# Optimization experiments

Hardware: AMD Instinct MI355X
Metric: run time of the kernel (lower is better)

Reference implementation:

```python
import jax, jax.numpy as jnp
import numpy as np

FOUR_PI = 4.0 * np.pi
INF_CLAMP = 1e30


def setup_inputs() -> dict:
    key = jax.random.key(0)
    k1, k2, k3, k4 = jax.random.split(key, 4)
    B, N, M, S = 16, 2048, 16, 128
    pcl_transformed = jax.random.normal(k1, (B, N, M, 3), dtype=jnp.float32)
    primitive_points = jax.random.normal(k2, (B, M, S, 3), dtype=jnp.float32)
    size = jax.random.uniform(k3, (B, M, 3), dtype=jnp.float32, minval=0.05, maxval=1.0)
    probs = jax.random.uniform(k4, (B, M), dtype=jnp.float32)
    return {"pcl_transformed": pcl_transformed, "primitive_points": primitive_points,
            "size": size, "probs": probs}


def reference(pcl_transformed, primitive_points, size, probs):
    B, N, M, _ = pcl_transformed.shape
    S = primitive_points.shape[2]

    # diff: (B, M, S, N, 3); dist: (B, M, S, N)
    diff = primitive_points[:, :, :, None, :] - jnp.transpose(pcl_transformed, (0, 2, 1, 3))[:, :, None, :, :]
    dist = jnp.sum(diff * diff, axis=-1)

    # ---- pcl_to_prim loss (min over S, sort over M, stick-breaking cumprod) ----
    d1 = jnp.transpose(jnp.min(dist, axis=2), (0, 2, 1))  # (B, N, M)
    idx = jnp.argsort(d1, axis=-1)                         # (B, N, M)
    distance = jnp.take_along_axis(d1, idx, axis=-1)
    p = jnp.take_along_axis(jnp.broadcast_to(probs[:, None, :], (B, N, M)), idx, axis=-1)
    neg_cumprod = jnp.cumprod(1.0 - p, axis=-1)
    neg_cumprod = jnp.concatenate([jnp.ones_like(neg_cumprod[..., :1]), neg_cumprod[..., :-1]], axis=-1)
    minprob = p * neg_cumprod
    pcl_to_prim = jnp.einsum('bnm,bnm->', distance, minprob) / (B * N)

    # ---- prim_to_pcl loss (min over N, superquadric-area weighting) ----
    d2 = jnp.min(dist, axis=-1)                            # (B, M, S)
    d2 = jnp.where(d2 >= INF_CLAMP, 0.0, d2)
    s0, s1, s2 = size[..., 0], size[..., 1], size[..., 2]
    area = FOUR_PI * ((s0 * s1) ** 1.6 / 3 + (s0 * s2) ** 1.6 / 3 + (s1 * s2) ** 1.6 / 3) ** 0.625
    area = M * area / jnp.sum(area, axis=-1, keepdims=True)  # (B, M)
    prim_to_pcl = jnp.einsum('bm,bm,bm->', jnp.mean(d2, axis=-1), probs, area) / (B * M)

    # No regularizer types enabled -> regs == 0 (matches regularizer_type=[]).
    regs = jnp.zeros((), dtype=pcl_to_prim.dtype)
    total = 1.0 * pcl_to_prim + 1.0 * prim_to_pcl + regs
    return total, pcl_to_prim, prim_to_pcl, regs
```

## Files before the change

kernel.cpp:

```cpp
#include <hip/hip_runtime.h>
#include <math.h>

#define BB 16
#define NN 2048
#define MM 16
#define SS 128

__constant__ const float kFourPi = 12.566370614359172f;

__global__ __launch_bounds__(1024, 4) void fused_dist_kernel(
    const float* __restrict__ pcl,
    const float* __restrict__ prim,
    float* __restrict__ d1,
    float* __restrict__ d2sum,
    unsigned int* __restrict__ counter)
{
    const int bi  = blockIdx.x;
    const int b   = ((bi & 7) << 1) | (bi >> 7);
    const int m   = (bi >> 3) & 15;
    const int bm  = (b << 4) | m;
    const int tid = threadIdx.x;

    __shared__ float  Qx[NN], Qy[NN], Qz[NN], Qh[NN];
    __shared__ float4 Plds[SS];
    __shared__ float  d1s[4][NN];
    __shared__ float  wred[16][64];
    __shared__ float  rsum[4];

    if (bi == 0 && tid == 0)
        __hip_atomic_store(counter, 0u, __ATOMIC_RELAXED, __HIP_MEMORY_SCOPE_AGENT);

    {
        const size_t base = ((size_t)(b * NN) * MM + m) * 3;
#pragma unroll
        for (int j = 0; j < 2; ++j) {
            const int n = tid + j * 1024;
            const float* q = pcl + base + (size_t)n * (MM * 3);
            const float x = q[0], y = q[1], z = q[2];
            Qx[n] = x; Qy[n] = y; Qz[n] = z;
            Qh[n] = 0.5f * (x * x + y * y + z * z);
        }
    }
    if (tid < SS) {
        const float* pp = prim + ((size_t)bm * SS + tid) * 3;
        const float x = pp[0], y = pp[1], z = pp[2];
        Plds[tid] = make_float4(x, y, z, 0.5f * (x * x + y * y + z * z));
    }
    __syncthreads();

    const int sub  = tid >> 8;
    const int stid = tid & 255;
    const int s0   = sub * 32;
    const int wid  = tid >> 6;
    const int lane = tid & 63;

    float qx[8], qy[8], qz[8], hq[8], d1m[8];
#pragma unroll
    for (int j = 0; j < 8; ++j) {
        const int n = stid + j * 256;
        qx[j] = Qx[n]; qy[j] = Qy[n]; qz[j] = Qz[n]; hq[j] = Qh[n];
        d1m[j] = 3.0e38f;
    }

    float d2r[32];
#pragma unroll
    for (int s = 0; s < 32; ++s) {
        const float4 f = Plds[s0 + s];
        float e[8];
#pragma unroll
        for (int j = 0; j < 8; ++j) {
            float t = hq[j] + f.w;
            t = fmaf(f.x, -qx[j], t);
            t = fmaf(f.y, -qy[j], t);
            t = fmaf(f.z, -qz[j], t);
            e[j] = t;
            d1m[j] = fminf(d1m[j], t);
        }
        const float m01 = fminf(e[0], e[1]);
        const float m23 = fminf(e[2], e[3]);
        const float m45 = fminf(e[4], e[5]);
        const float m67 = fminf(e[6], e[7]);
        d2r[s] = fminf(fminf(m01, m23), fminf(m45, m67));
    }

#pragma unroll
    for (int j = 0; j < 8; ++j)
        d1s[sub][stid + j * 256] = d1m[j];
    __syncthreads();
#pragma unroll
    for (int j = 0; j < 2; ++j) {
        const int n = tid + j * 1024;
        d1[(size_t)bm * NN + n] = fminf(fminf(d1s[0][n], d1s[1][n]),
                                        fminf(d1s[2][n], d1s[3][n]));
    }

    float v16[16];
    {
        const bool hi = (lane & 32) != 0;
#pragma unroll
        for (int k = 0; k < 16; ++k) {
            const float xk = hi ? d2r[k + 16] : d2r[k];
            const float xs = hi ? d2r[k] : d2r[k + 16];
            v16[k] = fminf(xk, __shfl_xor(xs, 32, 64));
        }
    }
    float v8[8];
    {
        const bool hi = (lane & 16) != 0;
#pragma unroll
        for (int k = 0; k < 8; ++k) {
            const float xk = hi ? v16[k + 8] : v16[k];
            const float xs = hi ? v16[k] : v16[k + 8];
            v8[k] = fminf(xk, __shfl_xor(xs, 16, 64));
        }
    }
    float v4[4];
    {
        const bool hi = (lane & 8) != 0;
#pragma unroll
        for (int k = 0; k < 4; ++k) {
            const float xk = hi ? v8[k + 4] : v8[k];
            const float xs = hi ? v8[k] : v8[k + 4];
            v4[k] = fminf(xk, __shfl_xor(xs, 8, 64));
        }
    }
    float v2a, v2b;
    {
        const bool hi = (lane & 4) != 0;
        const float xk0 = hi ? v4[2] : v4[0];
        const float xs0 = hi ? v4[0] : v4[2];
        v2a = fminf(xk0, __shfl_xor(xs0, 4, 64));
        const float xk1 = hi ? v4[3] : v4[1];
        const float xs1 = hi ? v4[1] : v4[3];
        v2b = fminf(xk1, __shfl_xor(xs1, 4, 64));
    }
    float v1;
    {
        const bool hi = (lane & 2) != 0;
        const float xk = hi ? v2b : v2a;
        const float xs = hi ? v2a : v2b;
        v1 = fminf(xk, __shfl_xor(xs, 2, 64));
    }
    const float r = fminf(v1, __shfl_xor(v1, 1, 64));
    wred[wid][lane] = r;
    __syncthreads();

    if (tid < 256) {
        const int sc = tid >> 6;
        const int l  = tid & 63;
        float mv = fminf(fminf(wred[sc * 4 + 0][l], wred[sc * 4 + 1][l]),
                         fminf(wred[sc * 4 + 2][l], wred[sc * 4 + 3][l]));
        if (mv >= 5.0e29f) mv = 0.0f;
#pragma unroll
        for (int off = 32; off > 0; off >>= 1)
            mv += __shfl_down(mv, off, 64);
        if (l == 0) rsum[sc] = mv;
    }
    __syncthreads();
    if (tid == 0) d2sum[bm] = rsum[0] + rsum[1] + rsum[2] + rsum[3];
}

__global__ __launch_bounds__(128) void p2p_final_kernel(
    const float* __restrict__ d1,
    const float* __restrict__ probs,
    const float* __restrict__ size_,
    const float* __restrict__ d2sum,
    float* __restrict__ partial,
    unsigned int* __restrict__ counter,
    float* __restrict__ out)
{
    const int tid = threadIdx.x;
    const int bi  = blockIdx.x;
    const int b   = ((bi & 7) << 1) | (bi >> 7);
    const int j   = (bi >> 3) & 15;
    const int n   = j * 128 + tid;

    float d[16], p[16];
#pragma unroll
    for (int m = 0; m < 16; ++m) {
        const float mn = d1[((size_t)(b * MM + m)) * NN + n];
        d[m] = mn + mn;
    }

    const float* pb = probs + b * MM;
#pragma unroll
    for (int k = 0; k < 16; ++k) p[k] = pb[k];

#define CE(i, jj)                                             \
    {                                                         \
        const bool c = d[i] > d[jj];                          \
        const float td = c ? d[jj] : d[i];                    \
        d[jj] = c ? d[i] : d[jj];  d[i] = td;                 \
        const float tp = c ? p[jj] : p[i];                    \
        p[jj] = c ? p[i] : p[jj];  p[i] = tp;                 \
    }
#pragma unroll
    for (int r = 0; r < 16; ++r) {
        if ((r & 1) == 0) {
            CE(0, 1) CE(2, 3) CE(4, 5) CE(6, 7)
            CE(8, 9) CE(10, 11) CE(12, 13) CE(14, 15)
        } else {
            CE(1, 2) CE(3, 4) CE(5, 6) CE(7, 8)
            CE(9, 10) CE(11, 12) CE(13, 14)
        }
    }
#undef CE

    float acc = 1.0f, sum = 0.0f;
#pragma unroll
    for (int k = 0; k < 16; ++k) {
        sum += d[k] * p[k] * acc;
        acc *= (1.0f - p[k]);
    }

    const int wid  = tid >> 6;
    const int lane = tid & 63;
    __shared__ float red2[2];
#pragma unroll
    for (int off = 32; off > 0; off >>= 1)
        sum += __shfl_down(sum, off, 64);
    if (lane == 0) red2[wid] = sum;
    __syncthreads();

    __shared__ bool amLast;
    if (tid == 0) {
        const float bsum = red2[0] + red2[1];
        __hip_atomic_store(&partial[bi], bsum,
                           __ATOMIC_RELEASE, __HIP_MEMORY_SCOPE_AGENT);
        const unsigned int prev = __hip_atomic_fetch_add(
            counter, 1u, __ATOMIC_ACQ_REL, __HIP_MEMORY_SCOPE_AGENT);
        amLast = (prev == 255u);
    }
    __syncthreads();
    if (!amLast) return;

    __shared__ float  areaSh[256];
    __shared__ double redA[2];
    __shared__ double redB[2];

#pragma unroll
    for (int k = 0; k < 2; ++k) {
        const int t = tid + k * 128;
        const float s0 = size_[t * 3 + 0];
        const float s1 = size_[t * 3 + 1];
        const float s2 = size_[t * 3 + 2];
        const float inner = powf(s0 * s1, 1.6f) * (1.0f / 3.0f)
                          + powf(s0 * s2, 1.6f) * (1.0f / 3.0f)
                          + powf(s1 * s2, 1.6f) * (1.0f / 3.0f);
        areaSh[t] = kFourPi * powf(inner, 0.625f);
    }
    __syncthreads();

    double t_acc = 0.0;
#pragma unroll
    for (int k = 0; k < 2; ++k) {
        const int t  = tid + k * 128;
        const int fb = t >> 4;
        float asum = 0.0f;
#pragma unroll
        for (int mm = 0; mm < 16; ++mm) asum += areaSh[fb * 16 + mm];
        const float anorm = 16.0f * areaSh[t] / asum;
        t_acc += (double)(d2sum[t] * (1.0f / 128.0f)) * (double)probs[t] * (double)anorm;
    }
#pragma unroll
    for (int off = 32; off > 0; off >>= 1)
        t_acc += __shfl_down(t_acc, off, 64);
    if (lane == 0) redA[wid] = t_acc;

    double u = 0.0;
    {
        const float pv0 = __hip_atomic_load(&partial[tid],
                                            __ATOMIC_ACQUIRE, __HIP_MEMORY_SCOPE_AGENT);
        const float pv1 = __hip_atomic_load(&partial[tid + 128],
                                            __ATOMIC_ACQUIRE, __HIP_MEMORY_SCOPE_AGENT);
        u = (double)pv0 + (double)pv1;
    }
#pragma unroll
    for (int off = 32; off > 0; off >>= 1)
        u += __shfl_down(u, off, 64);
    if (lane == 0) redB[wid] = u;

    __syncthreads();
    if (tid == 0) {
        const double prim_to_pcl = (redA[0] + redA[1]) / 256.0;
        const double pcl_to_prim = (redB[0] + redB[1]) / 32768.0;
        out[0] = (float)(pcl_to_prim + prim_to_pcl);
        out[1] = (float)pcl_to_prim;
        out[2] = (float)prim_to_pcl;
        out[3] = 0.0f;
    }
}


extern "C" void kernel_launch(void* const* d_in, const int* in_sizes, int n_in,
                              void* d_out, int out_size, void* d_ws, size_t ws_size,
                              hipStream_t stream) {
    const float* pcl   = (const float*)d_in[0];
    const float* prim  = (const float*)d_in[1];
    const float* size_ = (const float*)d_in[2];
    const float* probs = (const float*)d_in[3];
    float* out = (float*)d_out;

    float* d1             = (float*)d_ws;
    float* d2sum          = d1 + (size_t)256 * NN;
    float* partial        = d2sum + 256;
    unsigned int* counter = (unsigned int*)(partial + 256);

    fused_dist_kernel<<<BB * MM, 1024, 0, stream>>>(pcl, prim, d1, d2sum, counter);
    p2p_final_kernel<<<256, 128, 0, stream>>>(d1, probs, size_, d2sum, partial, counter, out);
}
```

Baseline: 88.06 us.

## Split point loading into two halves to overlap global loads with compute

The kernel now stages only the first 1024 points into LDS before the first barrier. The loads for the second half are issued early and held in registers while the first half's distance computation runs, then written to LDS behind a second barrier. The compute loop is split into two passes of 4 points each, with pairs of primitives per iteration. The intent is to hide global-load latency and lower register pressure, at the cost of an extra barrier and some d2 merging work.

```diff
diff --git a/kernel.cpp b/kernel.cpp
--- a/kernel.cpp
+++ b/kernel.cpp
@@ -30,23 +30,23 @@
     if (bi == 0 && tid == 0)
         __hip_atomic_store(counter, 0u, __ATOMIC_RELAXED, __HIP_MEMORY_SCOPE_AGENT);
 
-    {
-        const size_t base = ((size_t)(b * NN) * MM + m) * 3;
-#pragma unroll
-        for (int j = 0; j < 2; ++j) {
-            const int n = tid + j * 1024;
-            const float* q = pcl + base + (size_t)n * (MM * 3);
-            const float x = q[0], y = q[1], z = q[2];
-            Qx[n] = x; Qy[n] = y; Qz[n] = z;
-            Qh[n] = 0.5f * (x * x + y * y + z * z);
-        }
+    const size_t base = ((size_t)(b * NN) * MM + m) * 3;
+    {
+        const float* q = pcl + base + (size_t)tid * (MM * 3);
+        const float x = q[0], y = q[1], z = q[2];
+        Qx[tid] = x; Qy[tid] = y; Qz[tid] = z;
+        Qh[tid] = 0.5f * (x * x + y * y + z * z);
     }
     if (tid < SS) {
         const float* pp = prim + ((size_t)bm * SS + tid) * 3;
         const float x = pp[0], y = pp[1], z = pp[2];
         Plds[tid] = make_float4(x, y, z, 0.5f * (x * x + y * y + z * z));
     }
-    __syncthreads();
+    const float* q2p = pcl + base + (size_t)(tid + 1024) * (MM * 3);
+    const float x2 = q2p[0], y2 = q2p[1], z2 = q2p[2];
+
+    asm volatile("s_waitcnt lgkmcnt(0)" ::: "memory");
+    __builtin_amdgcn_s_barrier();
 
     const int sub  = tid >> 8;
     const int stid = tid & 255;
@@ -54,38 +54,78 @@
     const int wid  = tid >> 6;
     const int lane = tid & 63;
 
-    float qx[8], qy[8], qz[8], hq[8], d1m[8];
-#pragma unroll
-    for (int j = 0; j < 8; ++j) {
+    float qx[4], qy[4], qz[4], hq[4];
+    float d1mA[4], d1mB[4];
+    float d2r[32];
+
+#pragma unroll
+    for (int j = 0; j < 4; ++j) {
         const int n = stid + j * 256;
         qx[j] = Qx[n]; qy[j] = Qy[n]; qz[j] = Qz[n]; hq[j] = Qh[n];
-        d1m[j] = 3.0e38f;
-    }
-
-    float d2r[32];
-#pragma unroll
-    for (int s = 0; s < 32; ++s) {
-        const float4 f = Plds[s0 + s];
-        float e[8];
-#pragma unroll
-        for (int j = 0; j < 8; ++j) {
-            float t = hq[j] + f.w;
-            t = fmaf(f.x, -qx[j], t);
-            t = fmaf(f.y, -qy[j], t);
-            t = fmaf(f.z, -qz[j], t);
-            e[j] = t;
-            d1m[j] = fminf(d1m[j], t);
-        }
-        const float m01 = fminf(e[0], e[1]);
-        const float m23 = fminf(e[2], e[3]);
-        const float m45 = fminf(e[4], e[5]);
-        const float m67 = fminf(e[6], e[7]);
-        d2r[s] = fminf(fminf(m01, m23), fminf(m45, m67));
-    }
-
-#pragma unroll
-    for (int j = 0; j < 8; ++j)
-        d1s[sub][stid + j * 256] = d1m[j];
+        d1mA[j] = 3.0e38f;
+    }
+#pragma unroll
+    for (int sp = 0; sp < 16; ++sp) {
+        const float4 fa = Plds[s0 + 2 * sp];
+        const float4 fb = Plds[s0 + 2 * sp + 1];
+        float ea[4], eb[4];
+#pragma unroll
+        for (int j = 0; j < 4; ++j) {
+            float ta = hq[j] + fa.w;
+            ta = fmaf(fa.x, -qx[j], ta);
+            ta = fmaf(fa.y, -qy[j], ta);
+            ta = fmaf(fa.z, -qz[j], ta);
+            float tb = hq[j] + fb.w;
+            tb = fmaf(fb.x, -qx[j], tb);
+            tb = fmaf(fb.y, -qy[j], tb);
+            tb = fmaf(fb.z, -qz[j], tb);
+            ea[j] = ta; eb[j] = tb;
+            d1mA[j] = fminf(d1mA[j], fminf(ta, tb));
+        }
+        d2r[2 * sp]     = fminf(fminf(fminf(ea[0], ea[1]), ea[2]), ea[3]);
+        d2r[2 * sp + 1] = fminf(fminf(fminf(eb[0], eb[1]), eb[2]), eb[3]);
+    }
+
+    Qx[tid + 1024] = x2; Qy[tid + 1024] = y2; Qz[tid + 1024] = z2;
+    Qh[tid + 1024] = 0.5f * (x2 * x2 + y2 * y2 + z2 * z2);
+    asm volatile("s_waitcnt lgkmcnt(0)" ::: "memory");
+    __builtin_amdgcn_s_barrier();
+
+#pragma unroll
+    for (int j = 0; j < 4; ++j) {
+        const int n = 1024 + stid + j * 256;
+        qx[j] = Qx[n]; qy[j] = Qy[n]; qz[j] = Qz[n]; hq[j] = Qh[n];
+        d1mB[j] = 3.0e38f;
+    }
+#pragma unroll
+    for (int sp = 0; sp < 16; ++sp) {
+        const float4 fa = Plds[s0 + 2 * sp];
+        const float4 fb = Plds[s0 + 2 * sp + 1];
+        float ea[4], eb[4];
+#pragma unroll
+        for (int j = 0; j < 4; ++j) {
+            float ta = hq[j] + fa.w;
+            ta = fmaf(fa.x, -qx[j], ta);
+            ta = fmaf(fa.y, -qy[j], ta);
+            ta = fmaf(fa.z, -qz[j], ta);
+            float tb = hq[j] + fb.w;
+            tb = fmaf(fb.x, -qx[j], tb);
+            tb = fmaf(fb.y, -qy[j], tb);
+            tb = fmaf(fb.z, -qz[j], tb);
+            ea[j] = ta; eb[j] = tb;
+            d1mB[j] = fminf(d1mB[j], fminf(ta, tb));
+        }
+        d2r[2 * sp]     = fminf(fminf(fminf(fminf(ea[0], ea[1]), ea[2]), ea[3]),
+                                d2r[2 * sp]);
+        d2r[2 * sp + 1] = fminf(fminf(fminf(fminf(eb[0], eb[1]), eb[2]), eb[3]),
+                                d2r[2 * sp + 1]);
+    }
+
+#pragma unroll
+    for (int j = 0; j < 4; ++j) {
+        d1s[sub][stid + j * 256]        = d1mA[j];
+        d1s[sub][1024 + stid + j * 256] = d1mB[j];
+    }
     __syncthreads();
 #pragma unroll
     for (int j = 0; j < 2; ++j) {
```

After: 88.63 us. About the same (+0.7%).
